# Kernel tuning notes

Hardware: AMD Instinct MI355X
Metric: run time of the kernel (lower is better)

The kernel has to match this reference:

```python
import jax, jax.numpy as jnp
import numpy as np

V, E, D, B, C = 100000, 256, 128, 8192, 10  # vocab, embedding_size, context_size, batch, window


def setup_inputs() -> dict:
    key = jax.random.key(0)
    ks = jax.random.split(key, 11)
    s = 0.02
    return {
        "x": jax.random.randint(ks[0], (B,), 0, V),
        "context": jax.random.randint(ks[1], (B, C), 0, V),
        "W_emb": jax.random.normal(ks[2], (V, E), jnp.float32) * s,
        "M_w": jax.random.normal(ks[3], (D, E), jnp.float32) * s,
        "M_b": jnp.zeros((D,), jnp.float32),
        "U_w": jax.random.normal(ks[4], (D, 2 * D), jnp.float32) * s,
        "U_b": jnp.zeros((D,), jnp.float32),
        "W_w": jax.random.normal(ks[5], (D, 2 * D), jnp.float32) * s,
        "W_b": jnp.zeros((D,), jnp.float32),
        "prior_mus": jax.random.normal(ks[6], (V, D), jnp.float32) * s,
        # covariance diagonal must be positive for a valid Gaussian (torch would
        # Cholesky-fail otherwise); sample in [0.1, 1.0)
        "prior_sigmas": jax.random.uniform(ks[7], (V, D), jnp.float32, 0.1, 1.0),
    }


def reference(x, context, W_emb, M_w, M_b, U_w, U_b, W_w, W_b, prior_mus, prior_sigmas):
    emb_x = W_emb[x]                       # [B, E]
    emb_c = W_emb[context]                 # [B, C, E]
    Rw = emb_x @ M_w.T + M_b               # [B, D]  (repeated over C slots below)
    Rc = jnp.einsum('bce,de->bcd', emb_c, M_w) + M_b  # [B, C, D]
    RwC = jnp.broadcast_to(Rw[:, None, :], Rc.shape)   # repeat(len(context), 1)
    h = jax.nn.relu(jnp.concatenate([RwC, Rc], axis=-1)).sum(axis=1)  # [B, 2D]
    mu = h @ U_w.T + U_b                   # posterior mean  [B, D]
    sigma = jax.nn.softplus(h @ W_w.T + W_b)  # posterior cov diag [B, D]
    m0 = prior_mus[x]                      # prior mean      [B, D]
    s0 = prior_sigmas[x]                   # prior cov diag  [B, D]
    # closed-form KL(N(m0, diag(s0)) || N(mu, diag(sigma)))
    d = jnp.float32(D)
    kl = 0.5 * ((s0 / sigma).sum(-1)
                + ((mu - m0) ** 2 / sigma).sum(-1)
                - d
                + jnp.log(sigma).sum(-1) - jnp.log(s0).sum(-1))
    return kl  # [B]
```

## Files before the change

kernel.cpp:

```cpp
#include <hip/hip_runtime.h>
#include <hip/hip_bf16.h>
#include <math.h>


#define CTXN  10
#define DDIM  128
#define WS_M   0
#define WS_UW  32768
#define WS_H   98304

typedef short bf16x8 __attribute__((ext_vector_type(8)));
typedef float f32x4  __attribute__((ext_vector_type(4)));

__device__ __forceinline__ uint2 cvt4(float4 v) {
    union { __hip_bfloat162 h2; unsigned u; } a, b;
    a.h2 = __float22bfloat162_rn(make_float2(v.x, v.y));
    b.h2 = __float22bfloat162_rn(make_float2(v.z, v.w));
    return make_uint2(a.u, b.u);
}

__device__ __forceinline__ float softplusf(float v) {
    return fmaxf(v, 0.0f) + log1pf(expf(-fabsf(v)));
}

__global__ __launch_bounds__(256) void k_cvt(
    const float* __restrict__ M_w, const float* __restrict__ U_w,
    const float* __restrict__ W_w, unsigned short* __restrict__ ws)
{
    int which = blockIdx.x >> 5;
    int i = ((blockIdx.x & 31) << 8) | threadIdx.x;
    const float* src = (which == 0) ? M_w : (which == 1) ? U_w : W_w;
    float4 v = ((const float4*)src)[i];
    *(uint2*)&ws[which * 32768 + i * 4] = cvt4(v);
}

#define BT1   8
#define ROWS1 88
#define LP    72
#define ACH   (96 * LP)

__global__ __launch_bounds__(512, 4) void bsg_h(
    const int* __restrict__ x, const int* __restrict__ ctx,
    const float* __restrict__ W_emb, const float* __restrict__ M_b,
    const unsigned short* __restrict__ wsr, unsigned short* __restrict__ hws)
{
    __shared__ unsigned short A_s[2 * ACH];
    __shared__ int idx_s[ROWS1];

    const int tid  = threadIdx.x;
    const int b0   = blockIdx.x * BT1;
    const int w    = tid >> 6;
    const int lane = tid & 63;
    const int l15  = lane & 15;
    const int lg   = lane >> 4;

    if (tid < ROWS1) {
        int c = tid >> 3, b = b0 + (tid & 7);
        idx_s[tid] = (c == 0) ? x[b] : ctx[b * CTXN + (c - 1)];
    }

    const unsigned short* Mb_bf = wsr + WS_M;
    const int mrow = 16 * w + l15;
    bf16x8 mreg[8];
#pragma unroll
    for (int kk = 0; kk < 8; ++kk)
        mreg[kk] = *(const bf16x8*)&Mb_bf[mrow * 256 + 32 * kk + 8 * lg];

    __syncthreads();

    float4 rr[12];
#pragma unroll
    for (int ch = 0; ch < 4; ++ch)
#pragma unroll
        for (int s = 0; s < 3; ++s) {
            int it = tid + 512 * s;
            if (it < ROWS1 * 16) {
                int r = it >> 4, q = it & 15;
                rr[ch * 3 + s] =
                    ((const float4*)W_emb)[(size_t)idx_s[r] * 64 + ch * 16 + q];
            }
        }

    f32x4 acc[6] = {};
#pragma unroll
    for (int ch = 0; ch < 4; ++ch) {
        unsigned short* Ab = A_s + (ch & 1) * ACH;
#pragma unroll
        for (int s = 0; s < 3; ++s) {
            int it = tid + 512 * s;
            if (it < ROWS1 * 16) {
                int r = it >> 4, q = it & 15;
                *(uint2*)&Ab[r * LP + 4 * q] = cvt4(rr[ch * 3 + s]);
            }
        }
        __syncthreads();
        const unsigned short* Abr = A_s + (ch & 1) * ACH;
#pragma unroll
        for (int mt = 0; mt < 6; ++mt) {
            bf16x8 a0 = *(const bf16x8*)&Abr[(16 * mt + l15) * LP + 8 * lg];
            bf16x8 a1 = *(const bf16x8*)&Abr[(16 * mt + l15) * LP + 32 + 8 * lg];
            acc[mt] = __builtin_amdgcn_mfma_f32_16x16x32_bf16(a0, mreg[2 * ch],     acc[mt], 0, 0, 0);
            acc[mt] = __builtin_amdgcn_mfma_f32_16x16x32_bf16(a1, mreg[2 * ch + 1], acc[mt], 0, 0, 0);
        }
    }

    const int dg = 16 * w + l15;
    const float mb = M_b[dg];
    float p1[4] = {0, 0, 0, 0}, p2[4] = {0, 0, 0, 0};
#pragma unroll
    for (int mt = 0; mt < 6; ++mt) {
#pragma unroll
        for (int q = 0; q < 4; ++q) {
            float r = fmaxf(acc[mt][q] + mb, 0.0f);
            if (lg < 2) { if (mt == 0) p1[q] = r; else p2[q] += r; }
            else        { if (mt < 5)  p2[q] += r; }
        }
    }
#pragma unroll
    for (int q = 0; q < 4; ++q) {
        float other = __shfl_xor(p2[q], 32);
        if (lg < 2) {
            int b = 4 * lg + q;
            __hip_bfloat16 t1 = __float2bfloat16(10.0f * p1[q]);
            __hip_bfloat16 t2 = __float2bfloat16(p2[q] + other);
            hws[(size_t)(b0 + b) * 256 + dg]       = *(unsigned short*)&t1;
            hws[(size_t)(b0 + b) * 256 + 128 + dg] = *(unsigned short*)&t2;
        }
    }
}

#define BT2  16
#define HLP  264

__global__ __launch_bounds__(512, 4) void bsg_kl(
    const int* __restrict__ x, const float* __restrict__ U_b,
    const float* __restrict__ W_b, const float* __restrict__ pmu,
    const float* __restrict__ psg, const unsigned short* __restrict__ wsr,
    float* __restrict__ out)
{
    __shared__ unsigned short H_s[BT2 * HLP];
    __shared__ float P_s[BT2 * 8];

    const int tid  = threadIdx.x;
    const int b0   = blockIdx.x * BT2;
    const int w    = tid >> 6;
    const int lane = tid & 63;
    const int l15  = lane & 15;
    const int lg   = lane >> 4;
    const int d    = 16 * w + l15;

    float pm[4], ps[4];
#pragma unroll
    for (int q = 0; q < 4; ++q) {
        int xb = x[b0 + 4 * lg + q];
        pm[q] = pmu[(size_t)xb * DDIM + d];
        ps[q] = psg[(size_t)xb * DDIM + d];
    }

    const unsigned short* hws = wsr + WS_H;
    {
        int r = tid >> 5, q = tid & 31;
        *(uint4*)&H_s[r * HLP + 8 * q] =
            *(const uint4*)&hws[(size_t)(b0 + r) * 256 + 8 * q];
    }
    __syncthreads();

    const unsigned short* UWb = wsr + WS_UW;
    f32x4 acc2[2] = {};
#pragma unroll
    for (int ks = 0; ks < 8; ++ks) {
        bf16x8 hf = *(const bf16x8*)&H_s[l15 * HLP + 32 * ks + 8 * lg];
        bf16x8 bu = *(const bf16x8*)&UWb[d * 256 + 32 * ks + 8 * lg];
        bf16x8 bw = *(const bf16x8*)&UWb[(128 + d) * 256 + 32 * ks + 8 * lg];
        acc2[0] = __builtin_amdgcn_mfma_f32_16x16x32_bf16(hf, bu, acc2[0], 0, 0, 0);
        acc2[1] = __builtin_amdgcn_mfma_f32_16x16x32_bf16(hf, bw, acc2[1], 0, 0, 0);
    }

    const float ub = U_b[d], wb = W_b[d];
#pragma unroll
    for (int q = 0; q < 4; ++q) {
        int rb = 4 * lg + q;
        float mu = acc2[0][q] + ub;
        float sg = softplusf(acc2[1][q] + wb);
        float dm = mu - pm[q];
        float p  = ps[q] / sg + dm * dm / sg + logf(sg) - logf(ps[q]);
        p += __shfl_xor(p, 1);
        p += __shfl_xor(p, 2);
        p += __shfl_xor(p, 4);
        p += __shfl_xor(p, 8);
        if (l15 == 0) P_s[rb * 8 + w] = p;
    }
    __syncthreads();
    if (tid < BT2) {
        float s = 0.0f;
#pragma unroll
        for (int k = 0; k < 8; ++k) s += P_s[tid * 8 + k];
        out[b0 + tid] = 0.5f * (s - (float)DDIM);
    }
}

extern "C" void kernel_launch(void* const* d_in, const int* in_sizes, int n_in,
                              void* d_out, int out_size, void* d_ws, size_t ws_size,
                              hipStream_t stream) {
    const int*   x     = (const int*)  d_in[0];
    const int*   ctx   = (const int*)  d_in[1];
    const float* W_emb = (const float*)d_in[2];
    const float* M_w   = (const float*)d_in[3];
    const float* M_b   = (const float*)d_in[4];
    const float* U_w   = (const float*)d_in[5];
    const float* U_b   = (const float*)d_in[6];
    const float* W_w   = (const float*)d_in[7];
    const float* W_b   = (const float*)d_in[8];
    const float* pmu   = (const float*)d_in[9];
    const float* psg   = (const float*)d_in[10];
    float* out = (float*)d_out;
    unsigned short* ws = (unsigned short*)d_ws;

    k_cvt<<<dim3(96), dim3(256), 0, stream>>>(M_w, U_w, W_w, ws);
    bsg_h<<<dim3(8192 / BT1), dim3(512), 0, stream>>>(x, ctx, W_emb, M_b,
                                                      ws, ws + WS_H);
    bsg_kl<<<dim3(8192 / BT2), dim3(512), 0, stream>>>(x, U_b, W_b, pmu, psg,
                                                       ws, out);
}
```

Baseline: 47.91 us.

## Precompute ReLU projected embeddings for whole vocabulary, then gather bf16 rows

Replaces the per-batch gather-then-project kernel with a dense pass that computes relu(W_emb·M_wᵀ + M_b) for every vocabulary row, stored as bf16. The KL kernel now gathers these 128-wide bf16 rows per token and sums the context slots itself to build h. This trades random 1KB fp32 row gathers for a streaming read of the full embedding table plus a 256-byte bf16 gather per token. It also writes an extra vocab-sized intermediate to workspace and projects rows that no token uses.

```diff
diff --git a/kernel.cpp b/kernel.cpp
--- a/kernel.cpp
+++ b/kernel.cpp
@@ -5,9 +5,10 @@
 
 #define CTXN  10
 #define DDIM  128
+#define VNUM  100000
 #define WS_M   0
 #define WS_UW  32768
-#define WS_H   98304
+#define WS_R   98304
 
 typedef short bf16x8 __attribute__((ext_vector_type(8)));
 typedef float f32x4  __attribute__((ext_vector_type(4)));
@@ -17,6 +18,16 @@
     a.h2 = __float22bfloat162_rn(make_float2(v.x, v.y));
     b.h2 = __float22bfloat162_rn(make_float2(v.z, v.w));
     return make_uint2(a.u, b.u);
+}
+
+__device__ __forceinline__ float bf2f(unsigned short s) {
+    union { unsigned u; float f; } t; t.u = (unsigned)s << 16; return t.f;
+}
+
+__device__ __forceinline__ unsigned packbf2(float a, float b) {
+    union { __hip_bfloat162 h2; unsigned u; } t;
+    t.h2 = __float22bfloat162_rn(make_float2(a, b));
+    return t.u;
 }
 
 __device__ __forceinline__ float softplusf(float v) {
@@ -34,111 +45,102 @@
     *(uint2*)&ws[which * 32768 + i * 4] = cvt4(v);
 }
 
-#define BT1   8
-#define ROWS1 88
-#define LP    72
-#define ACH   (96 * LP)
-
-__global__ __launch_bounds__(512, 4) void bsg_h(
-    const int* __restrict__ x, const int* __restrict__ ctx,
+#define RROWS 128
+#define LPA   72
+#define ACHA  (RROWS * LPA)
+#define LPR   136
+
+__device__ __forceinline__ void loadWE(const float4* __restrict__ We, int v0,
+                                       int rbase, int rq, int ch, float4* dst) {
+#pragma unroll
+    for (int s = 0; s < 4; ++s) {
+        int vr = v0 + rbase + 32 * s;
+        vr = (vr < VNUM) ? vr : (VNUM - 1);
+        dst[s] = We[(size_t)vr * 64 + ch * 16 + rq];
+    }
+}
+__device__ __forceinline__ void writeA(unsigned short* Ab, int rbase, int rq,
+                                       const float4* src) {
+#pragma unroll
+    for (int s = 0; s < 4; ++s)
+        *(uint2*)&Ab[(rbase + 32 * s) * LPA + 4 * rq] = cvt4(src[s]);
+}
+
+__global__ __launch_bounds__(512, 4) void k_prer(
     const float* __restrict__ W_emb, const float* __restrict__ M_b,
-    const unsigned short* __restrict__ wsr, unsigned short* __restrict__ hws)
+    const unsigned short* __restrict__ wsr, unsigned short* __restrict__ Rout)
 {
-    __shared__ unsigned short A_s[2 * ACH];
-    __shared__ int idx_s[ROWS1];
+    __shared__ __align__(16) unsigned short A_s[2 * ACHA];
 
     const int tid  = threadIdx.x;
-    const int b0   = blockIdx.x * BT1;
+    const int v0   = blockIdx.x * RROWS;
     const int w    = tid >> 6;
     const int lane = tid & 63;
     const int l15  = lane & 15;
     const int lg   = lane >> 4;
 
-    if (tid < ROWS1) {
-        int c = tid >> 3, b = b0 + (tid & 7);
-        idx_s[tid] = (c == 0) ? x[b] : ctx[b * CTXN + (c - 1)];
-    }
-
-    const unsigned short* Mb_bf = wsr + WS_M;
+    const int rq    = tid & 15;
+    const int rbase = tid >> 4;
+
+    const float4* We = (const float4*)W_emb;
+    float4 rr0[4], rr1[4];
+    loadWE(We, v0, rbase, rq, 0, rr0);
+    loadWE(We, v0, rbase, rq, 1, rr1);
+
+    const unsigned short* Mb = wsr + WS_M;
     const int mrow = 16 * w + l15;
-    bf16x8 mreg[8];
-#pragma unroll
-    for (int kk = 0; kk < 8; ++kk)
-        mreg[kk] = *(const bf16x8*)&Mb_bf[mrow * 256 + 32 * kk + 8 * lg];
-
-    __syncthreads();
-
-    float4 rr[12];
-#pragma unroll
-    for (int ch = 0; ch < 4; ++ch)
-#pragma unroll
-        for (int s = 0; s < 3; ++s) {
-            int it = tid + 512 * s;
-            if (it < ROWS1 * 16) {
-                int r = it >> 4, q = it & 15;
-                rr[ch * 3 + s] =
-                    ((const float4*)W_emb)[(size_t)idx_s[r] * 64 + ch * 16 + q];
-            }
+    f32x4 acc[8] = {};
+
+#pragma unroll
+    for (int ch = 0; ch < 4; ++ch) {
+        unsigned short* Ab = A_s + (ch & 1) * ACHA;
+        if (ch & 1) { writeA(Ab, rbase, rq, rr1); if (ch < 2) loadWE(We, v0, rbase, rq, ch + 2, rr1); }
+        else        { writeA(Ab, rbase, rq, rr0); if (ch < 2) loadWE(We, v0, rbase, rq, ch + 2, rr0); }
+        __syncthreads();
+        bf16x8 m0 = *(const bf16x8*)&Mb[mrow * 256 + 64 * ch + 8 * lg];
+        bf16x8 m1 = *(const bf16x8*)&Mb[mrow * 256 + 64 * ch + 32 + 8 * lg];
+        const unsigned short* Abr = A_s + (ch & 1) * ACHA;
+#pragma unroll
+        for (int mt = 0; mt < 8; ++mt) {
+            bf16x8 a0 = *(const bf16x8*)&Abr[(16 * mt + l15) * LPA + 8 * lg];
+            bf16x8 a1 = *(const bf16x8*)&Abr[(16 * mt + l15) * LPA + 32 + 8 * lg];
+            acc[mt] = __builtin_amdgcn_mfma_f32_16x16x32_bf16(a0, m0, acc[mt], 0, 0, 0);
+            acc[mt] = __builtin_amdgcn_mfma_f32_16x16x32_bf16(a1, m1, acc[mt], 0, 0, 0);
         }
-
-    f32x4 acc[6] = {};
-#pragma unroll
-    for (int ch = 0; ch < 4; ++ch) {
-        unsigned short* Ab = A_s + (ch & 1) * ACH;
-#pragma unroll
-        for (int s = 0; s < 3; ++s) {
-            int it = tid + 512 * s;
-            if (it < ROWS1 * 16) {
-                int r = it >> 4, q = it & 15;
-                *(uint2*)&Ab[r * LP + 4 * q] = cvt4(rr[ch * 3 + s]);
-            }
-        }
-        __syncthreads();
-        const unsigned short* Abr = A_s + (ch & 1) * ACH;
-#pragma unroll
-        for (int mt = 0; mt < 6; ++mt) {
-            bf16x8 a0 = *(const bf16x8*)&Abr[(16 * mt + l15) * LP + 8 * lg];
-            bf16x8 a1 = *(const bf16x8*)&Abr[(16 * mt + l15) * LP + 32 + 8 * lg];
-            acc[mt] = __builtin_amdgcn_mfma_f32_16x16x32_bf16(a0, mreg[2 * ch],     acc[mt], 0, 0, 0);
-            acc[mt] = __builtin_amdgcn_mfma_f32_16x16x32_bf16(a1, mreg[2 * ch + 1], acc[mt], 0, 0, 0);
-        }
-    }
-
-    const int dg = 16 * w + l15;
-    const float mb = M_b[dg];
-    float p1[4] = {0, 0, 0, 0}, p2[4] = {0, 0, 0, 0};
-#pragma unroll
-    for (int mt = 0; mt < 6; ++mt) {
+    }
+
+    __syncthreads();
+    unsigned short* R_s = A_s;
+    const float mb = M_b[16 * w + l15];
+#pragma unroll
+    for (int mt = 0; mt < 8; ++mt)
 #pragma unroll
         for (int q = 0; q < 4; ++q) {
             float r = fmaxf(acc[mt][q] + mb, 0.0f);
-            if (lg < 2) { if (mt == 0) p1[q] = r; else p2[q] += r; }
-            else        { if (mt < 5)  p2[q] += r; }
+            __hip_bfloat16 t = __float2bfloat16(r);
+            R_s[(16 * mt + 4 * lg + q) * LPR + 16 * w + l15] = *(unsigned short*)&t;
         }
-    }
-#pragma unroll
-    for (int q = 0; q < 4; ++q) {
-        float other = __shfl_xor(p2[q], 32);
-        if (lg < 2) {
-            int b = 4 * lg + q;
-            __hip_bfloat16 t1 = __float2bfloat16(10.0f * p1[q]);
-            __hip_bfloat16 t2 = __float2bfloat16(p2[q] + other);
-            hws[(size_t)(b0 + b) * 256 + dg]       = *(unsigned short*)&t1;
-            hws[(size_t)(b0 + b) * 256 + 128 + dg] = *(unsigned short*)&t2;
-        }
+    __syncthreads();
+#pragma unroll
+    for (int s = 0; s < 4; ++s) {
+        int it = tid + 512 * s;
+        int row = it >> 4, q = it & 15;
+        if (v0 + row < VNUM)
+            *(uint4*)&Rout[(size_t)(v0 + row) * 128 + 8 * q] =
+                *(const uint4*)&R_s[row * LPR + 8 * q];
     }
 }
 
 #define BT2  16
 #define HLP  264
 
-__global__ __launch_bounds__(512, 4) void bsg_kl(
-    const int* __restrict__ x, const float* __restrict__ U_b,
-    const float* __restrict__ W_b, const float* __restrict__ pmu,
-    const float* __restrict__ psg, const unsigned short* __restrict__ wsr,
-    float* __restrict__ out)
+__global__ __launch_bounds__(512, 4) void bsg_kl2(
+    const int* __restrict__ x, const int* __restrict__ ctx,
+    const float* __restrict__ U_b, const float* __restrict__ W_b,
+    const float* __restrict__ pmu, const float* __restrict__ psg,
+    const unsigned short* __restrict__ wsr, float* __restrict__ out)
 {
-    __shared__ unsigned short H_s[BT2 * HLP];
+    __shared__ __align__(16) unsigned short H_s[BT2 * HLP];
     __shared__ float P_s[BT2 * 8];
 
     const int tid  = threadIdx.x;
@@ -157,11 +159,42 @@
         ps[q] = psg[(size_t)xb * DDIM + d];
     }
 
-    const unsigned short* hws = wsr + WS_H;
+    const int g    = tid >> 5;
+    const int t    = tid & 31;
+    const int half = t >> 4;
+    const int dk   = t & 15;
+    const int b    = b0 + g;
+    const unsigned short* R = wsr + WS_R;
+
+    float hacc[8] = {0, 0, 0, 0, 0, 0, 0, 0};
+#pragma unroll
+    for (int k = 0; k < 5; ++k) {
+        int ci = ctx[b * CTXN + 2 * k + half];
+        uint4 rv = *(const uint4*)&R[(size_t)ci * 128 + 8 * dk];
+        union { uint4 u; unsigned short s[8]; } uv; uv.u = rv;
+#pragma unroll
+        for (int j = 0; j < 8; ++j) hacc[j] += bf2f(uv.s[j]);
+    }
+    float vals[8];
+    if (half == 0) {
+        int xb = x[b];
+        uint4 rx = *(const uint4*)&R[(size_t)xb * 128 + 8 * dk];
+        union { uint4 u; unsigned short s[8]; } uv; uv.u = rx;
+#pragma unroll
+        for (int j = 0; j < 8; ++j) vals[j] = 10.0f * bf2f(uv.s[j]);
+    }
+#pragma unroll
+    for (int j = 0; j < 8; ++j) {
+        float tot = hacc[j] + __shfl_xor(hacc[j], 16);
+        if (half) vals[j] = tot;
+    }
     {
-        int r = tid >> 5, q = tid & 31;
-        *(uint4*)&H_s[r * HLP + 8 * q] =
-            *(const uint4*)&hws[(size_t)(b0 + r) * 256 + 8 * q];
+        uint4 pk;
+        pk.x = packbf2(vals[0], vals[1]);
+        pk.y = packbf2(vals[2], vals[3]);
+        pk.z = packbf2(vals[4], vals[5]);
+        pk.w = packbf2(vals[6], vals[7]);
+        *(uint4*)&H_s[g * HLP + half * 128 + 8 * dk] = pk;
     }
     __syncthreads();
 
@@ -217,8 +250,8 @@
     unsigned short* ws = (unsigned short*)d_ws;
 
     k_cvt<<<dim3(96), dim3(256), 0, stream>>>(M_w, U_w, W_w, ws);
-    bsg_h<<<dim3(8192 / BT1), dim3(512), 0, stream>>>(x, ctx, W_emb, M_b,
-                                                      ws, ws + WS_H);
-    bsg_kl<<<dim3(8192 / BT2), dim3(512), 0, stream>>>(x, U_b, W_b, pmu, psg,
-                                                       ws, out);
-}
+    k_prer<<<dim3((VNUM + RROWS - 1) / RROWS), dim3(512), 0, stream>>>(
+        W_emb, M_b, ws, ws + WS_R);
+    bsg_kl2<<<dim3(8192 / BT2), dim3(512), 0, stream>>>(
+        x, ctx, U_b, W_b, pmu, psg, ws, out);
+}
```

New measurement: 53.59 us. 1.12x slower.
